# Kernel tuning notes

Hardware: AMD Instinct MI355X
Metric: run time of the kernel (lower is better)

## Reference

```python
import jax, jax.numpy as jnp
import numpy as np
from jax.scipy.special import gammaln, xlogy

B, T, C = 1, 1536, 1536
H, K, V = 8, 64, 192   # heads, key size per head, value size per head (C // H)
F = 192                # num_relative_position_features (C // H)
LN_EPS = 1e-3          # keras LayerNormalization default


def _layer_norm(x, g, b):
    mu = jnp.mean(x, axis=-1, keepdims=True)
    var = jnp.var(x, axis=-1, keepdims=True)
    return (x - mu) * jax.lax.rsqrt(var + LN_EPS) * g + b


def _positional_features(positions, feature_size, seq_length):
    # 3 symmetric basis classes x 2 (symmetric + sign-asymmetric) = 6 components
    n = feature_size // 6
    ap = jnp.abs(positions)[:, None]  # [L, 1]
    # exponential half-life decay
    half_life = (2.0 ** np.linspace(3.0, np.log2(seq_length), n)).astype(np.float32)
    f_exp = jnp.exp(ap * (-(np.log(2.0) / half_life))[None, :].astype(np.float32))
    # central mask
    widths = (2.0 ** np.arange(1, n + 1) - 1.0).astype(np.float32)
    f_cm = (widths[None, :] > ap).astype(jnp.float32)
    # gamma pdf bumps
    stddev = seq_length / (2.0 * n)
    mean = np.linspace(seq_length / n, float(seq_length), n)
    conc = ((mean / stddev) ** 2).astype(np.float32)
    rate = (mean / stddev ** 2).astype(np.float32)
    log_unnorm = xlogy(conc - 1.0, ap) - rate * ap
    log_norm = (gammaln(conc) - conc * np.log(rate)).astype(np.float32)
    prob = jnp.exp(log_unnorm - log_norm) + 1e-8
    f_g = prob / jnp.max(prob, axis=1, keepdims=True)
    emb = jnp.concatenate([f_exp, f_cm, f_g], axis=-1)          # [L, F/2]
    emb = jnp.concatenate([emb, jnp.sign(positions)[:, None] * emb], axis=-1)
    return emb                                                   # [L, F]


def _relative_shift(x):
    # TransformerXL shift: [B,H,T,2T-1] -> [B,H,T,T]
    b, h, t1, t2 = x.shape
    x = jnp.pad(x, ((0, 0), (0, 0), (0, 0), (1, 0)))
    x = x.reshape(b, h, t2 + 1, t1)[:, :, 1:, :].reshape(b, h, t1, t2)
    return x[..., :(t2 + 1) // 2]


def _forward(x, ln1_g, ln1_b, ln2_g, ln2_b, Wq, Wk, Wv, Wr, Wo, bo,
             r_w_bias, r_r_bias, W1, b1, W2, b2):
    Bv, Tv, Cv = x.shape
    # --- multi-head attention with relative positions ---
    xn = _layer_norm(x, ln1_g, ln1_b)
    q = (xn @ Wq).reshape(Bv, Tv, H, K).transpose(0, 2, 1, 3) * (K ** -0.5)
    k = (xn @ Wk).reshape(Bv, Tv, H, K).transpose(0, 2, 1, 3)
    v = (xn @ Wv).reshape(Bv, Tv, H, V).transpose(0, 2, 1, 3)
    content = jnp.einsum('bhqk,bhmk->bhqm', q + r_w_bias, k)     # [B,H,T,T]
    distances = jnp.arange(-Tv + 1, Tv, dtype=jnp.float32)       # [2T-1]
    pos = _positional_features(distances, F, Tv)                 # [2T-1, F]
    r_k = (pos @ Wr).reshape(2 * Tv - 1, H, K).transpose(1, 0, 2)
    rel = jnp.einsum('bhqk,hmk->bhqm', q + r_r_bias, r_k)        # [B,H,T,2T-1]
    logits = content + _relative_shift(rel)
    attn = jax.nn.softmax(logits, axis=-1)
    o = jnp.einsum('bhqm,bhmv->bhqv', attn, v)
    o = o.transpose(0, 2, 1, 3).reshape(Bv, Tv, H * V) @ Wo + bo
    y = x + o
    # --- MLP ---
    yn = _layer_norm(y, ln2_g, ln2_b)
    h1 = jax.nn.relu(yn @ W1 + b1)
    return y + h1 @ W2 + b2


def setup_inputs() -> dict:
    key = jax.random.key(0)
    ks = jax.random.split(key, 10)
    nrm = lambda i, shape, s=0.02: jax.random.normal(ks[i], shape, jnp.float32) * s
    return {
        'x': jax.random.normal(ks[0], (B, T, C), jnp.float32),
        'ln1_g': jnp.ones((C,), jnp.float32), 'ln1_b': jnp.zeros((C,), jnp.float32),
        'ln2_g': jnp.ones((C,), jnp.float32), 'ln2_b': jnp.zeros((C,), jnp.float32),
        'Wq': nrm(1, (C, H * K)), 'Wk': nrm(2, (C, H * K)), 'Wv': nrm(3, (C, H * V)),
        'Wr': nrm(4, (F, H * K)), 'Wo': nrm(5, (H * V, C)),
        'bo': jnp.zeros((C,), jnp.float32),
        'r_w_bias': nrm(6, (1, H, 1, K), 0.1), 'r_r_bias': nrm(7, (1, H, 1, K), 0.1),
        'W1': nrm(8, (C, 2 * C)), 'b1': jnp.zeros((2 * C,), jnp.float32),
        'W2': nrm(9, (2 * C, C)), 'b2': jnp.zeros((C,), jnp.float32),
    }


def reference(x, ln1_g, ln1_b, ln2_g, ln2_b, Wq, Wk, Wv, Wr, Wo, bo,
              r_w_bias, r_r_bias, W1, b1, W2, b2):
    return _forward(x, ln1_g, ln1_b, ln2_g, ln2_b, Wq, Wk, Wv, Wr, Wo, bo,
                    r_w_bias, r_r_bias, W1, b1, W2, b2)
```

## Files before the change

kernel.cpp:

```cpp
#include <hip/hip_runtime.h>
#include <math.h>

#define TT 1536
#define CC 1536
#define NH 8
#define KD 64
#define VD 192
#define FD 192

typedef short bf16x8 __attribute__((ext_vector_type(8)));
typedef float f32x4 __attribute__((ext_vector_type(4)));

__device__ inline unsigned short f2bf(float x) {
    unsigned u = __float_as_uint(x);
    u += 0x7FFF + ((u >> 16) & 1);
    return (unsigned short)(u >> 16);
}
__device__ inline float bf2f(unsigned short b) {
    return __uint_as_float(((unsigned)b) << 16);
}
__device__ inline void gload16(const void* g, void* l) {
    __builtin_amdgcn_global_load_lds(
        (const __attribute__((address_space(1))) unsigned int*)g,
        (__attribute__((address_space(3))) unsigned int*)l, 16, 0, 0);
}
__device__ inline int swzo(int row, int chunk) { return (chunk ^ (row & 7)) << 3; }

template<int N> __device__ inline void vmwait() {
    if constexpr (N == 0)      asm volatile("s_waitcnt vmcnt(0)" ::: "memory");
    else if constexpr (N == 4) asm volatile("s_waitcnt vmcnt(4)" ::: "memory");
    else if constexpr (N == 6) asm volatile("s_waitcnt vmcnt(6)" ::: "memory");
    else                       asm volatile("s_waitcnt vmcnt(8)" ::: "memory");
}

__global__ __launch_bounds__(256)
void ln_kernel(const float* __restrict__ x, const float* __restrict__ g,
               const float* __restrict__ b, unsigned short* __restrict__ out)
{
    int row = blockIdx.x;
    int tid = threadIdx.x;
    const float* xr = x + (size_t)row * CC;
    unsigned short* orow = out + (size_t)row * CC;

    float vals[6];
    float s = 0.f, ss = 0.f;
#pragma unroll
    for (int i = 0; i < 6; i++) {
        float v = xr[tid + i * 256];
        vals[i] = v;
        s += v; ss += v * v;
    }
    __shared__ float red[256], red2[256];
    red[tid] = s; red2[tid] = ss;
    __syncthreads();
    for (int off = 128; off > 0; off >>= 1) {
        if (tid < off) { red[tid] += red[tid + off]; red2[tid] += red2[tid + off]; }
        __syncthreads();
    }
    float mean = red[0] * (1.f / CC);
    float var  = red2[0] * (1.f / CC) - mean * mean;
    float rstd = rsqrtf(fmaxf(var, 0.f) + 1e-3f);
#pragma unroll
    for (int i = 0; i < 6; i++) {
        int c = tid + i * 256;
        orow[c] = f2bf((vals[i] - mean) * rstd * g[c] + b[c]);
    }
}

struct WCD { const float* W; unsigned short* Wt; int Kw, Nw, t0; };
struct WCP { WCD e[7]; };

__global__ __launch_bounds__(256)
void wconv_all(WCP p)
{
    __shared__ float t[32][33];
    int bid = blockIdx.x;
    int i = 0;
#pragma unroll
    for (int j = 1; j < 7; j++) if (bid >= p.e[j].t0) i = j;
    const float* W = p.e[i].W;
    unsigned short* Wt = p.e[i].Wt;
    int Kw = p.e[i].Kw, Nw = p.e[i].Nw;
    int local = bid - p.e[i].t0;
    int tpx = Nw >> 5;
    int n0 = (local % tpx) * 32, k0 = (local / tpx) * 32;

    int tid = threadIdx.x;
    int r = tid >> 3, c4 = (tid & 7) * 4;
    float4 v = *reinterpret_cast<const float4*>(&W[(size_t)(k0 + r) * Nw + n0 + c4]);
    t[r][c4 + 0] = v.x; t[r][c4 + 1] = v.y; t[r][c4 + 2] = v.z; t[r][c4 + 3] = v.w;
    __syncthreads();
    ushort4 pk;
    pk.x = f2bf(t[c4 + 0][r]);
    pk.y = f2bf(t[c4 + 1][r]);
    pk.z = f2bf(t[c4 + 2][r]);
    pk.w = f2bf(t[c4 + 3][r]);
    *reinterpret_cast<ushort4*>(&Wt[(size_t)(n0 + r) * Kw + k0 + c4]) = pk;
}

__global__ __launch_bounds__(128)
void pos_kernel(unsigned short* __restrict__ pos)
{
    int l = blockIdx.x;
    int tid = threadIdx.x;
    float p = (float)(l - (TT - 1));
    float ap = fabsf(p);
    float sgn = (p > 0.f) ? 1.f : ((p < 0.f) ? -1.f : 0.f);

    __shared__ float gp[32];
    __shared__ float gmax_s;
    if (tid < 32) {
        int j = tid;
        double conc = 4.0 * (double)(j + 1) * (double)(j + 1);
        double rate = (double)(j + 1) / 12.0;
        double log_norm = lgamma(conc) - conc * log(rate);
        double prob;
        if (ap == 0.f) prob = 1e-8;
        else prob = exp((conc - 1.0) * log((double)ap) - rate * (double)ap - log_norm) + 1e-8;
        gp[j] = (float)prob;
    }
    __syncthreads();
    if (tid == 0) {
        float m = gp[0];
        for (int j = 1; j < 32; j++) m = fmaxf(m, gp[j]);
        gmax_s = m;
    }
    __syncthreads();
    if (tid < 96) {
        int cls = tid / 32, j = tid % 32;
        float val;
        if (cls == 0) {
            double step = (10.584962500721156 - 3.0) / 31.0;
            double hl = exp2(3.0 + j * step);
            val = (float)exp(-(double)ap * 0.6931471805599453 / hl);
        } else if (cls == 1) {
            float width = exp2f((float)(j + 1)) - 1.f;
            val = (width > ap) ? 1.f : 0.f;
        } else {
            val = gp[j] / gmax_s;
        }
        pos[(size_t)l * FD + tid] = f2bf(val);
        pos[(size_t)l * FD + 96 + tid] = f2bf(sgn * val);
    }
}

template<int TM, int TN>
__global__ __launch_bounds__(256)
void gemm_bf16(const unsigned short* __restrict__ A,
               const unsigned short* __restrict__ Bt,
               void* __restrict__ Cv, unsigned short* __restrict__ C2,
               unsigned short* __restrict__ C3,
               int M, int N, int K, int lda, int ldb, int ldc,
               long sA, long sB, long sC,
               float alpha, const float* __restrict__ bias,
               const float* __restrict__ bias2,
               const float* __restrict__ resid,
               int mode, int relu, int head_ndiv, int xm)
{
    constexpr int WM = TM / 2, WN = TN / 2;
    constexpr int MF = WM / 16, NF = WN / 16;
    constexpr int LPT = TM / 32 + TN / 32;
    __shared__ unsigned short lA[2][TM * 64];
    __shared__ unsigned short lB[2][TN * 64];

    int tid = threadIdx.x;
    int w = tid >> 6, l = tid & 63;

    int gx = gridDim.x, gy = gridDim.y;
    int d = blockIdx.y * gx + blockIdx.x;
    int bx, by;
    if (xm) {
        int xn = 8 / xm;
        int cm = gy / xm, cn = gx / xn;
        int xcd = d & 7, local = d >> 3;
        int bxl = local / cm, byl = local % cm;
        by = (xcd / xn) * cm + byl;
        bx = (xcd % xn) * cn + bxl;
    } else {
        int nwg = gx * gy;
        int work = d;
        if ((nwg & 7) == 0) work = (d & 7) * (nwg >> 3) + (d >> 3);
        bx = work % gx;
        by = work / gx;
    }

    int n0 = bx * TN;
    int m0 = by * TM;
    if (head_ndiv) {
        A += (size_t)(n0 / head_ndiv) * sA;
    } else {
        A  += (size_t)blockIdx.z * sA;
        Bt += (size_t)blockIdx.z * sB;
    }
    int R0 = (w & 1) * WM, C0 = (w >> 1) * WN;
    int lrow = l >> 3;
    int lsw = ((l & 7) ^ lrow) << 3;
    int l15 = l & 15, lg = l >> 4;

    f32x4 acc[MF][NF] = {};

    const int NSTEP = K >> 6;

    auto STAGE = [&](int t, int buf) {
        int k0 = t << 6;
#pragma unroll
        for (int q = 0; q < TM / 32; q++) {
            int r0 = w * (TM / 4) + q * 8;
            gload16(A + (size_t)(m0 + r0 + lrow) * lda + k0 + lsw, &lA[buf][r0 * 64]);
        }
#pragma unroll
        for (int q = 0; q < TN / 32; q++) {
            int r0 = w * (TN / 4) + q * 8;
            gload16(Bt + (size_t)(n0 + r0 + lrow) * ldb + k0 + lsw, &lB[buf][r0 * 64]);
        }
    };

    STAGE(0, 0);

    int cur = 0;
    for (int t = 0; t < NSTEP; ++t) {
        if (t + 1 < NSTEP) {
            STAGE(t + 1, cur ^ 1);
            vmwait<LPT>();
        } else {
            vmwait<0>();
        }
        __builtin_amdgcn_s_barrier();
        __builtin_amdgcn_sched_barrier(0);

#pragma unroll
        for (int kk = 0; kk < 2; kk++) {
            int ch = kk * 4 + lg;
            bf16x8 av[MF], bv[NF];
#pragma unroll
            for (int m = 0; m < MF; m++) {
                int row = R0 + m * 16 + l15;
                av[m] = *(const bf16x8*)&lA[cur][row * 64 + swzo(row, ch)];
            }
#pragma unroll
            for (int n = 0; n < NF; n++) {
                int row = C0 + n * 16 + l15;
                bv[n] = *(const bf16x8*)&lB[cur][row * 64 + swzo(row, ch)];
            }
#pragma unroll
            for (int m = 0; m < MF; m++)
#pragma unroll
                for (int n = 0; n < NF; n++)
                    acc[m][n] = __builtin_amdgcn_mfma_f32_16x16x32_bf16(av[m], bv[n], acc[m][n], 0, 0, 0);
        }
        __builtin_amdgcn_s_barrier();
        cur ^= 1;
    }

    int rb = m0 + R0 + lg * 4;
    int cb = n0 + C0 + l15;

    if (mode == 4) {
        unsigned short* qw = (unsigned short*)Cv;
#pragma unroll
        for (int m = 0; m < MF; m++) {
            int rowb = rb + m * 16;
#pragma unroll
            for (int n = 0; n < NF; n++) {
                int col = cb + n * 16;
                if (col < 512) {
#pragma unroll
                    for (int reg = 0; reg < 4; reg++) {
                        int row = rowb + reg;
                        float v = alpha * acc[m][n][reg];
                        qw[(size_t)row * 512 + col] = f2bf(v + bias[col]);
                        C2[(size_t)row * 512 + col] = f2bf(v + bias2[col]);
                    }
                } else if (col < 1024) {
                    unsigned short* kb = C3;
#pragma unroll
                    for (int reg = 0; reg < 4; reg++)
                        kb[(size_t)(rowb + reg) * 512 + col - 512] = f2bf(acc[m][n][reg]);
                } else {
                    unsigned short* vT = (unsigned short*)(void*)(C3 + (size_t)1536 * 512);
                    int vc = col - 1024;
                    ushort4 pk;
                    pk.x = f2bf(acc[m][n][0]);
                    pk.y = f2bf(acc[m][n][1]);
                    pk.z = f2bf(acc[m][n][2]);
                    pk.w = f2bf(acc[m][n][3]);
                    *reinterpret_cast<ushort4*>(&vT[(size_t)vc * 1536 + rowb]) = pk;
                }
            }
        }
        return;
    }

#pragma unroll
    for (int m = 0; m < MF; m++) {
#pragma unroll
        for (int n = 0; n < NF; n++) {
            int col = cb + n * 16;
            if (col >= N) continue;
            float bs = bias ? bias[col] : 0.f;
#pragma unroll
            for (int reg = 0; reg < 4; reg++) {
                int row = rb + m * 16 + reg;
                if (row >= M) continue;
                float v = alpha * acc[m][n][reg] + bs;
                if (resid) v += resid[(size_t)row * ldc + col];
                if (relu)  v = fmaxf(v, 0.f);
                if (mode == 1) {
                    unsigned short* C = (unsigned short*)Cv + (size_t)blockIdx.z * sC;
                    C[(size_t)row * ldc + col] = f2bf(v);
                } else {
                    float* C = (float*)Cv + (size_t)blockIdx.z * sC;
                    C[(size_t)row * ldc + col] = v;
                }
            }
        }
    }
}

__global__ __launch_bounds__(256)
void logits_mfma(const unsigned short* __restrict__ qw,
                 const unsigned short* __restrict__ qr,
                 const unsigned short* __restrict__ kmat,
                 const unsigned short* __restrict__ rk,
                 unsigned short* __restrict__ out)
{
    __shared__ unsigned short pool[3 * 64 * 64 + 128 * 64];
    unsigned short* lQw = pool;
    unsigned short* lQr = pool + 64 * 64;
    unsigned short* lK  = pool + 2 * 64 * 64;
    unsigned short* lR  = pool + 3 * 64 * 64;
    unsigned short* lC2 = pool;

    int j0 = blockIdx.x * 64;
    int i0 = blockIdx.y * 64;
    int h  = blockIdx.z;
    int tid = threadIdx.x;
    int w = tid >> 6, l = tid & 63;
    int lrow = l >> 3;
    int lsw = ((l & 7) ^ lrow) << 3;
    int l15 = l & 15, lg = l >> 4;
    int obase = j0 - i0 + 1472;

#pragma unroll
    for (int q = 0; q < 2; q++) {
        int r0 = w * 16 + q * 8;
        gload16(qw   + (size_t)(i0 + r0 + lrow) * (NH * KD) + h * KD + lsw, &lQw[r0 * 64]);
        gload16(qr   + (size_t)(i0 + r0 + lrow) * (NH * KD) + h * KD + lsw, &lQr[r0 * 64]);
        gload16(kmat + (size_t)(j0 + r0 + lrow) * (NH * KD) + h * KD + lsw, &lK [r0 * 64]);
    }
#pragma unroll
    for (int q = 0; q < 4; q++) {
        int r0 = w * 32 + q * 8;
        gload16(rk + (size_t)(obase + r0 + lrow) * (NH * KD) + h * KD + lsw, &lR[r0 * 64]);
    }
    __syncthreads();

    f32x4 acc1[4] = {};
    f32x4 acc2[8] = {};
#pragma unroll
    for (int kk = 0; kk < 2; kk++) {
        int ch = kk * 4 + lg;
        int qrow = 16 * w + l15;
        bf16x8 av  = *(const bf16x8*)&lQw[qrow * 64 + swzo(qrow, ch)];
        bf16x8 arv = *(const bf16x8*)&lQr[qrow * 64 + swzo(qrow, ch)];
#pragma unroll
        for (int n = 0; n < 4; n++) {
            int row = n * 16 + l15;
            bf16x8 bv = *(const bf16x8*)&lK[row * 64 + swzo(row, ch)];
            acc1[n] = __builtin_amdgcn_mfma_f32_16x16x32_bf16(av, bv, acc1[n], 0, 0, 0);
        }
#pragma unroll
        for (int n = 0; n < 8; n++) {
            int row = n * 16 + l15;
            bf16x8 rv = *(const bf16x8*)&lR[row * 64 + swzo(row, ch)];
            acc2[n] = __builtin_amdgcn_mfma_f32_16x16x32_bf16(arv, rv, acc2[n], 0, 0, 0);
        }
    }
    __syncthreads();

#pragma unroll
    for (int n = 0; n < 8; n++)
#pragma unroll
        for (int reg = 0; reg < 4; reg++)
            lC2[(16 * w + lg * 4 + reg) * 128 + n * 16 + l15] = f2bf(acc2[n][reg]);
    __syncthreads();

#pragma unroll
    for (int n = 0; n < 4; n++) {
#pragma unroll
        for (int reg = 0; reg < 4; reg++) {
            int u = 16 * w + lg * 4 + reg;
            int v = n * 16 + l15;
            float val = acc1[n][reg] + bf2f(lC2[u * 128 + 63 + v - u]);
            out[((size_t)h * TT + i0 + u) * TT + j0 + v] = f2bf(val);
        }
    }
}

__global__ __launch_bounds__(256)
void softmax_bf16(unsigned short* __restrict__ P)
{
    int r = blockIdx.x;
    int tid = threadIdx.x;
    unsigned* row = (unsigned*)(P + (size_t)r * TT);

    unsigned u[3]; float v[6];
#pragma unroll
    for (int i = 0; i < 3; i++) u[i] = row[tid + i * 256];
    float m = -1e30f;
#pragma unroll
    for (int i = 0; i < 3; i++) {
        v[2 * i]     = bf2f((unsigned short)(u[i] & 0xFFFF));
        v[2 * i + 1] = bf2f((unsigned short)(u[i] >> 16));
        m = fmaxf(m, fmaxf(v[2 * i], v[2 * i + 1]));
    }
    __shared__ float red[256];
    red[tid] = m; __syncthreads();
    for (int off = 128; off > 0; off >>= 1) {
        if (tid < off) red[tid] = fmaxf(red[tid], red[tid + off]);
        __syncthreads();
    }
    m = red[0];
    __syncthreads();
    float s = 0.f;
#pragma unroll
    for (int i = 0; i < 6; i++) { v[i] = __expf(v[i] - m); s += v[i]; }
    red[tid] = s; __syncthreads();
    for (int off = 128; off > 0; off >>= 1) {
        if (tid < off) red[tid] += red[tid + off];
        __syncthreads();
    }
    float inv = 1.f / red[0];
#pragma unroll
    for (int i = 0; i < 3; i++)
        row[tid + i * 256] = (unsigned)f2bf(v[2 * i] * inv)
                           | ((unsigned)f2bf(v[2 * i + 1] * inv) << 16);
}

extern "C" void kernel_launch(void* const* d_in, const int* in_sizes, int n_in,
                              void* d_out, int out_size, void* d_ws, size_t ws_size,
                              hipStream_t stream)
{
    const float* x     = (const float*)d_in[0];
    const float* ln1_g = (const float*)d_in[1];
    const float* ln1_b = (const float*)d_in[2];
    const float* ln2_g = (const float*)d_in[3];
    const float* ln2_b = (const float*)d_in[4];
    const float* Wq    = (const float*)d_in[5];
    const float* Wk    = (const float*)d_in[6];
    const float* Wv    = (const float*)d_in[7];
    const float* Wr    = (const float*)d_in[8];
    const float* Wo    = (const float*)d_in[9];
    const float* bo    = (const float*)d_in[10];
    const float* rwb   = (const float*)d_in[11];
    const float* rrb   = (const float*)d_in[12];
    const float* W1    = (const float*)d_in[13];
    const float* b1    = (const float*)d_in[14];
    const float* W2    = (const float*)d_in[15];
    const float* b2    = (const float*)d_in[16];
    float* out = (float*)d_out;

    char* w8 = (char*)d_ws;
    unsigned short* xnb  = (unsigned short*)(w8 + 0);
    unsigned short* qwb  = (unsigned short*)(w8 + 4718592);
    unsigned short* qrb  = (unsigned short*)(w8 + 6291456);
    unsigned short* kbb  = (unsigned short*)(w8 + 7864320);
    unsigned short* vTb  = (unsigned short*)(w8 + 9437184);
    unsigned short* posb = (unsigned short*)(w8 + 14155776);
    unsigned short* rkb  = (unsigned short*)(w8 + 15335424);
    unsigned short* Pb   = (unsigned short*)(w8 + 18481152);
    unsigned short* ob   = (unsigned short*)(w8 + 56229888);
    float*          yb   = (float*)        (w8 + 60948480);
    unsigned short* WqkvT= (unsigned short*)(w8 + 70385664);
    unsigned short* WrT  = (unsigned short*)(w8 + 78249984);
    unsigned short* WoT  = (unsigned short*)(w8 + 78446592);
    unsigned short* W1T  = (unsigned short*)(w8 + 83165184);
    unsigned short* W2T  = (unsigned short*)(w8 + 92602368);
    unsigned short* h1b  = Pb;
    unsigned short* ynb  = xnb;

    WCP wp;
    wp.e[0] = { Wq, WqkvT,                       1536, 512,      0 };
    wp.e[1] = { Wk, WqkvT + (size_t)512 * 1536,  1536, 512,    768 };
    wp.e[2] = { Wv, WqkvT + (size_t)1024 * 1536, 1536, 1536,  1536 };
    wp.e[3] = { Wr, WrT,                          192, 512,   3840 };
    wp.e[4] = { Wo, WoT,                         1536, 1536,  3936 };
    wp.e[5] = { W1, W1T,                         1536, 3072,  6240 };
    wp.e[6] = { W2, W2T,                         3072, 1536, 10848 };
    wconv_all<<<15456, 256, 0, stream>>>(wp);

    ln_kernel<<<TT, 256, 0, stream>>>(x, ln1_g, ln1_b, xnb);
    pos_kernel<<<2 * TT - 1, 128, 0, stream>>>(posb);

    gemm_bf16<64, 128><<<dim3(20, 24, 1), 256, 0, stream>>>(xnb, WqkvT, qwb, qrb, kbb,
        1536, 2560, 1536, 1536, 1536, 0, 0, 0, 0,
        0.125f, rwb, rrb, nullptr, 4, 0, 0, 2);

    gemm_bf16<64, 128><<<dim3(4, 48, 1), 256, 0, stream>>>(posb, WrT, rkb, nullptr, nullptr,
        3071, 512, 192, 192, 192, 512, 0, 0, 0,
        1.f, nullptr, nullptr, nullptr, 1, 0, 0, 2);

    logits_mfma<<<dim3(24, 24, 8), 256, 0, stream>>>(qwb, qrb, kbb, rkb, Pb);
    softmax_bf16<<<NH * TT, 256, 0, stream>>>(Pb);

    gemm_bf16<64, 64><<<dim3(24, 24, 1), 256, 0, stream>>>(Pb, vTb, ob, nullptr, nullptr,
        1536, 1536, 1536, 1536, 1536, 1536, (long)TT * TT, 0, 0,
        1.f, nullptr, nullptr, nullptr, 1, 0, VD, 2);

    gemm_bf16<64, 64><<<dim3(24, 24, 1), 256, 0, stream>>>(ob, WoT, yb, nullptr, nullptr,
        1536, 1536, 1536, 1536, 1536, 1536, 0, 0, 0,
        1.f, bo, nullptr, x, 0, 0, 0, 2);

    ln_kernel<<<TT, 256, 0, stream>>>(yb, ln2_g, ln2_b, ynb);

    gemm_bf16<64, 128><<<dim3(24, 24, 1), 256, 0, stream>>>(ynb, W1T, h1b, nullptr, nullptr,
        1536, 3072, 1536, 1536, 1536, 3072, 0, 0, 0,
        1.f, b1, nullptr, nullptr, 1, 1, 0, 2);

    gemm_bf16<64, 64><<<dim3(24, 24, 1), 256, 0, stream>>>(h1b, W2T, out, nullptr, nullptr,
        1536, 1536, 3072, 3072, 3072, 1536, 0, 0, 0,
        1.f, b2, nullptr, yb, 0, 0, 0, 4);
}
```

Baseline: 217.9 us.

## Add triple-buffered LDS pipeline to bf16 GEMM and shrink all tiles to 64x64

```diff
diff --git a/kernel.cpp b/kernel.cpp
--- a/kernel.cpp
+++ b/kernel.cpp
@@ -27,10 +27,12 @@
 __device__ inline int swzo(int row, int chunk) { return (chunk ^ (row & 7)) << 3; }
 
 template<int N> __device__ inline void vmwait() {
-    if constexpr (N == 0)      asm volatile("s_waitcnt vmcnt(0)" ::: "memory");
-    else if constexpr (N == 4) asm volatile("s_waitcnt vmcnt(4)" ::: "memory");
-    else if constexpr (N == 6) asm volatile("s_waitcnt vmcnt(6)" ::: "memory");
-    else                       asm volatile("s_waitcnt vmcnt(8)" ::: "memory");
+    if constexpr (N == 0)       asm volatile("s_waitcnt vmcnt(0)" ::: "memory");
+    else if constexpr (N == 4)  asm volatile("s_waitcnt vmcnt(4)" ::: "memory");
+    else if constexpr (N == 6)  asm volatile("s_waitcnt vmcnt(6)" ::: "memory");
+    else if constexpr (N == 8)  asm volatile("s_waitcnt vmcnt(8)" ::: "memory");
+    else if constexpr (N == 12) asm volatile("s_waitcnt vmcnt(12)" ::: "memory");
+    else                        asm volatile("s_waitcnt vmcnt(0)" ::: "memory");
 }
 
 __global__ __launch_bounds__(256)
@@ -144,7 +146,7 @@
     }
 }
 
-template<int TM, int TN>
+template<int TM, int TN, int DEPTH>
 __global__ __launch_bounds__(256)
 void gemm_bf16(const unsigned short* __restrict__ A,
                const unsigned short* __restrict__ Bt,
@@ -160,8 +162,8 @@
     constexpr int WM = TM / 2, WN = TN / 2;
     constexpr int MF = WM / 16, NF = WN / 16;
     constexpr int LPT = TM / 32 + TN / 32;
-    __shared__ unsigned short lA[2][TM * 64];
-    __shared__ unsigned short lB[2][TN * 64];
+    __shared__ unsigned short lA[DEPTH][TM * 64];
+    __shared__ unsigned short lB[DEPTH][TN * 64];
 
     int tid = threadIdx.x;
     int w = tid >> 6, l = tid & 63;
@@ -216,11 +218,14 @@
     };
 
     STAGE(0, 0);
-
-    int cur = 0;
+    if (DEPTH >= 3 && NSTEP > 1) STAGE(1, 1);
+
     for (int t = 0; t < NSTEP; ++t) {
-        if (t + 1 < NSTEP) {
-            STAGE(t + 1, cur ^ 1);
+        int cur = t % DEPTH;
+        if (t + DEPTH - 1 < NSTEP) {
+            STAGE(t + DEPTH - 1, (t + DEPTH - 1) % DEPTH);
+            vmwait<(DEPTH - 1) * LPT>();
+        } else if (DEPTH >= 3 && t + 1 < NSTEP) {
             vmwait<LPT>();
         } else {
             vmwait<0>();
@@ -249,7 +254,6 @@
                     acc[m][n] = __builtin_amdgcn_mfma_f32_16x16x32_bf16(av[m], bv[n], acc[m][n], 0, 0, 0);
         }
         __builtin_amdgcn_s_barrier();
-        cur ^= 1;
     }
 
     int rb = m0 + R0 + lg * 4;
@@ -492,32 +496,32 @@
     ln_kernel<<<TT, 256, 0, stream>>>(x, ln1_g, ln1_b, xnb);
     pos_kernel<<<2 * TT - 1, 128, 0, stream>>>(posb);
 
-    gemm_bf16<64, 128><<<dim3(20, 24, 1), 256, 0, stream>>>(xnb, WqkvT, qwb, qrb, kbb,
+    gemm_bf16<64, 64, 3><<<dim3(40, 24, 1), 256, 0, stream>>>(xnb, WqkvT, qwb, qrb, kbb,
         1536, 2560, 1536, 1536, 1536, 0, 0, 0, 0,
         0.125f, rwb, rrb, nullptr, 4, 0, 0, 2);
 
-    gemm_bf16<64, 128><<<dim3(4, 48, 1), 256, 0, stream>>>(posb, WrT, rkb, nullptr, nullptr,
+    gemm_bf16<64, 64, 3><<<dim3(8, 48, 1), 256, 0, stream>>>(posb, WrT, rkb, nullptr, nullptr,
         3071, 512, 192, 192, 192, 512, 0, 0, 0,
         1.f, nullptr, nullptr, nullptr, 1, 0, 0, 2);
 
     logits_mfma<<<dim3(24, 24, 8), 256, 0, stream>>>(qwb, qrb, kbb, rkb, Pb);
     softmax_bf16<<<NH * TT, 256, 0, stream>>>(Pb);
 
-    gemm_bf16<64, 64><<<dim3(24, 24, 1), 256, 0, stream>>>(Pb, vTb, ob, nullptr, nullptr,
+    gemm_bf16<64, 64, 3><<<dim3(24, 24, 1), 256, 0, stream>>>(Pb, vTb, ob, nullptr, nullptr,
         1536, 1536, 1536, 1536, 1536, 1536, (long)TT * TT, 0, 0,
         1.f, nullptr, nullptr, nullptr, 1, 0, VD, 2);
 
-    gemm_bf16<64, 64><<<dim3(24, 24, 1), 256, 0, stream>>>(ob, WoT, yb, nullptr, nullptr,
+    gemm_bf16<64, 64, 3><<<dim3(24, 24, 1), 256, 0, stream>>>(ob, WoT, yb, nullptr, nullptr,
         1536, 1536, 1536, 1536, 1536, 1536, 0, 0, 0,
         1.f, bo, nullptr, x, 0, 0, 0, 2);
 
     ln_kernel<<<TT, 256, 0, stream>>>(yb, ln2_g, ln2_b, ynb);
 
-    gemm_bf16<64, 128><<<dim3(24, 24, 1), 256, 0, stream>>>(ynb, W1T, h1b, nullptr, nullptr,
+    gemm_bf16<64, 64, 3><<<dim3(48, 24, 1), 256, 0, stream>>>(ynb, W1T, h1b, nullptr, nullptr,
         1536, 3072, 1536, 1536, 1536, 3072, 0, 0, 0,
         1.f, b1, nullptr, nullptr, 1, 1, 0, 2);
 
-    gemm_bf16<64, 64><<<dim3(24, 24, 1), 256, 0, stream>>>(h1b, W2T, out, nullptr, nullptr,
+    gemm_bf16<64, 64, 3><<<dim3(24, 24, 1), 256, 0, stream>>>(h1b, W2T, out, nullptr, nullptr,
         1536, 1536, 3072, 3072, 3072, 1536, 0, 0, 0,
         1.f, b2, nullptr, yb, 0, 0, 0, 4);
 }
```

New measurement: 233.5 us. 7.1% more time.

## Merge prep kernels and use wave-per-row layernorm and softmax

Applied to the files above, without the earlier changes.

```diff
diff --git a/kernel.cpp b/kernel.cpp
--- a/kernel.cpp
+++ b/kernel.cpp
@@ -33,114 +33,139 @@
     else                       asm volatile("s_waitcnt vmcnt(8)" ::: "memory");
 }
 
+__device__ inline void ln_row(const float* __restrict__ x,
+                              const float* __restrict__ g,
+                              const float* __restrict__ b,
+                              unsigned short* __restrict__ out,
+                              int row, int lane)
+{
+    const float* xr = x + (size_t)row * CC;
+    unsigned short* orow = out + (size_t)row * CC;
+
+    float4 V[6];
+    float s = 0.f, ss = 0.f;
+#pragma unroll
+    for (int c = 0; c < 6; c++) {
+        V[c] = *reinterpret_cast<const float4*>(&xr[c * 256 + lane * 4]);
+        s  += V[c].x + V[c].y + V[c].z + V[c].w;
+        ss += V[c].x * V[c].x + V[c].y * V[c].y + V[c].z * V[c].z + V[c].w * V[c].w;
+    }
+#pragma unroll
+    for (int off = 32; off; off >>= 1) {
+        s  += __shfl_xor(s, off);
+        ss += __shfl_xor(ss, off);
+    }
+    float mean = s * (1.f / CC);
+    float var  = ss * (1.f / CC) - mean * mean;
+    float rstd = rsqrtf(fmaxf(var, 0.f) + 1e-3f);
+#pragma unroll
+    for (int c = 0; c < 6; c++) {
+        float4 G = *reinterpret_cast<const float4*>(&g[c * 256 + lane * 4]);
+        float4 B = *reinterpret_cast<const float4*>(&b[c * 256 + lane * 4]);
+        ushort4 pk;
+        pk.x = f2bf((V[c].x - mean) * rstd * G.x + B.x);
+        pk.y = f2bf((V[c].y - mean) * rstd * G.y + B.y);
+        pk.z = f2bf((V[c].z - mean) * rstd * G.z + B.z);
+        pk.w = f2bf((V[c].w - mean) * rstd * G.w + B.w);
+        *reinterpret_cast<ushort4*>(&orow[c * 256 + lane * 4]) = pk;
+    }
+}
+
 __global__ __launch_bounds__(256)
 void ln_kernel(const float* __restrict__ x, const float* __restrict__ g,
                const float* __restrict__ b, unsigned short* __restrict__ out)
 {
-    int row = blockIdx.x;
-    int tid = threadIdx.x;
-    const float* xr = x + (size_t)row * CC;
-    unsigned short* orow = out + (size_t)row * CC;
-
-    float vals[6];
-    float s = 0.f, ss = 0.f;
-#pragma unroll
-    for (int i = 0; i < 6; i++) {
-        float v = xr[tid + i * 256];
-        vals[i] = v;
-        s += v; ss += v * v;
-    }
-    __shared__ float red[256], red2[256];
-    red[tid] = s; red2[tid] = ss;
-    __syncthreads();
-    for (int off = 128; off > 0; off >>= 1) {
-        if (tid < off) { red[tid] += red[tid + off]; red2[tid] += red2[tid + off]; }
-        __syncthreads();
-    }
-    float mean = red[0] * (1.f / CC);
-    float var  = red2[0] * (1.f / CC) - mean * mean;
-    float rstd = rsqrtf(fmaxf(var, 0.f) + 1e-3f);
-#pragma unroll
-    for (int i = 0; i < 6; i++) {
-        int c = tid + i * 256;
-        orow[c] = f2bf((vals[i] - mean) * rstd * g[c] + b[c]);
-    }
+    int wid = threadIdx.x >> 6, lane = threadIdx.x & 63;
+    ln_row(x, g, b, out, blockIdx.x * 4 + wid, lane);
 }
 
 struct WCD { const float* W; unsigned short* Wt; int Kw, Nw, t0; };
 struct WCP { WCD e[7]; };
+#define WCONV_BLKS 15456
+#define LN1_BLKS   384
+#define POS_BLKS   (2 * TT - 1)
 
 __global__ __launch_bounds__(256)
-void wconv_all(WCP p)
-{
-    __shared__ float t[32][33];
+void prep_all(WCP p, const float* __restrict__ x,
+              const float* __restrict__ ln1_g, const float* __restrict__ ln1_b,
+              unsigned short* __restrict__ xnb, unsigned short* __restrict__ pos)
+{
     int bid = blockIdx.x;
-    int i = 0;
-#pragma unroll
-    for (int j = 1; j < 7; j++) if (bid >= p.e[j].t0) i = j;
-    const float* W = p.e[i].W;
-    unsigned short* Wt = p.e[i].Wt;
-    int Kw = p.e[i].Kw, Nw = p.e[i].Nw;
-    int local = bid - p.e[i].t0;
-    int tpx = Nw >> 5;
-    int n0 = (local % tpx) * 32, k0 = (local / tpx) * 32;
-
     int tid = threadIdx.x;
-    int r = tid >> 3, c4 = (tid & 7) * 4;
-    float4 v = *reinterpret_cast<const float4*>(&W[(size_t)(k0 + r) * Nw + n0 + c4]);
-    t[r][c4 + 0] = v.x; t[r][c4 + 1] = v.y; t[r][c4 + 2] = v.z; t[r][c4 + 3] = v.w;
-    __syncthreads();
-    ushort4 pk;
-    pk.x = f2bf(t[c4 + 0][r]);
-    pk.y = f2bf(t[c4 + 1][r]);
-    pk.z = f2bf(t[c4 + 2][r]);
-    pk.w = f2bf(t[c4 + 3][r]);
-    *reinterpret_cast<ushort4*>(&Wt[(size_t)(n0 + r) * Kw + k0 + c4]) = pk;
-}
-
-__global__ __launch_bounds__(128)
-void pos_kernel(unsigned short* __restrict__ pos)
-{
-    int l = blockIdx.x;
-    int tid = threadIdx.x;
-    float p = (float)(l - (TT - 1));
-    float ap = fabsf(p);
-    float sgn = (p > 0.f) ? 1.f : ((p < 0.f) ? -1.f : 0.f);
-
-    __shared__ float gp[32];
-    __shared__ float gmax_s;
-    if (tid < 32) {
-        int j = tid;
-        double conc = 4.0 * (double)(j + 1) * (double)(j + 1);
-        double rate = (double)(j + 1) / 12.0;
-        double log_norm = lgamma(conc) - conc * log(rate);
-        double prob;
-        if (ap == 0.f) prob = 1e-8;
-        else prob = exp((conc - 1.0) * log((double)ap) - rate * (double)ap - log_norm) + 1e-8;
-        gp[j] = (float)prob;
-    }
-    __syncthreads();
-    if (tid == 0) {
-        float m = gp[0];
-        for (int j = 1; j < 32; j++) m = fmaxf(m, gp[j]);
-        gmax_s = m;
-    }
-    __syncthreads();
-    if (tid < 96) {
-        int cls = tid / 32, j = tid % 32;
-        float val;
-        if (cls == 0) {
-            double step = (10.584962500721156 - 3.0) / 31.0;
-            double hl = exp2(3.0 + j * step);
-            val = (float)exp(-(double)ap * 0.6931471805599453 / hl);
-        } else if (cls == 1) {
-            float width = exp2f((float)(j + 1)) - 1.f;
-            val = (width > ap) ? 1.f : 0.f;
-        } else {
-            val = gp[j] / gmax_s;
-        }
-        pos[(size_t)l * FD + tid] = f2bf(val);
-        pos[(size_t)l * FD + 96 + tid] = f2bf(sgn * val);
+
+    if (bid < WCONV_BLKS) {
+        __shared__ float t[32][33];
+        int i = 0;
+#pragma unroll
+        for (int j = 1; j < 7; j++) if (bid >= p.e[j].t0) i = j;
+        const float* W = p.e[i].W;
+        unsigned short* Wt = p.e[i].Wt;
+        int Kw = p.e[i].Kw, Nw = p.e[i].Nw;
+        int local = bid - p.e[i].t0;
+        int tpx = Nw >> 5;
+        int n0 = (local % tpx) * 32, k0 = (local / tpx) * 32;
+
+        int r = tid >> 3, c4 = (tid & 7) * 4;
+        float4 v = *reinterpret_cast<const float4*>(&W[(size_t)(k0 + r) * Nw + n0 + c4]);
+        t[r][c4 + 0] = v.x; t[r][c4 + 1] = v.y; t[r][c4 + 2] = v.z; t[r][c4 + 3] = v.w;
+        __syncthreads();
+        ushort4 pk;
+        pk.x = f2bf(t[c4 + 0][r]);
+        pk.y = f2bf(t[c4 + 1][r]);
+        pk.z = f2bf(t[c4 + 2][r]);
+        pk.w = f2bf(t[c4 + 3][r]);
+        *reinterpret_cast<ushort4*>(&Wt[(size_t)(n0 + r) * Kw + k0 + c4]) = pk;
+        return;
+    }
+
+    if (bid < WCONV_BLKS + LN1_BLKS) {
+        int grp = bid - WCONV_BLKS;
+        int wid = tid >> 6, lane = tid & 63;
+        ln_row(x, ln1_g, ln1_b, xnb, grp * 4 + wid, lane);
+        return;
+    }
+
+    {
+        int l = bid - (WCONV_BLKS + LN1_BLKS);
+        float pp = (float)(l - (TT - 1));
+        float ap = fabsf(pp);
+        float sgn = (pp > 0.f) ? 1.f : ((pp < 0.f) ? -1.f : 0.f);
+
+        __shared__ float gp[32];
+        __shared__ float gmax_s;
+        if (tid < 32) {
+            int j = tid;
+            double conc = 4.0 * (double)(j + 1) * (double)(j + 1);
+            double rate = (double)(j + 1) / 12.0;
+            double log_norm = lgamma(conc) - conc * log(rate);
+            double prob;
+            if (ap == 0.f) prob = 1e-8;
+            else prob = exp((conc - 1.0) * log((double)ap) - rate * (double)ap - log_norm) + 1e-8;
+            gp[j] = (float)prob;
+        }
+        __syncthreads();
+        if (tid == 0) {
+            float m = gp[0];
+            for (int j = 1; j < 32; j++) m = fmaxf(m, gp[j]);
+            gmax_s = m;
+        }
+        __syncthreads();
+        if (tid < 96) {
+            int cls = tid / 32, j = tid % 32;
+            float val;
+            if (cls == 0) {
+                double step = (10.584962500721156 - 3.0) / 31.0;
+                double hl = exp2(3.0 + j * step);
+                val = (float)exp(-(double)ap * 0.6931471805599453 / hl);
+            } else if (cls == 1) {
+                float width = exp2f((float)(j + 1)) - 1.f;
+                val = (width > ap) ? 1.f : 0.f;
+            } else {
+                val = gp[j] / gmax_s;
+            }
+            pos[(size_t)l * FD + tid] = f2bf(val);
+            pos[(size_t)l * FD + 96 + tid] = f2bf(sgn * val);
+        }
     }
 }
 
@@ -400,41 +425,43 @@
 __global__ __launch_bounds__(256)
 void softmax_bf16(unsigned short* __restrict__ P)
 {
-    int r = blockIdx.x;
-    int tid = threadIdx.x;
-    unsigned* row = (unsigned*)(P + (size_t)r * TT);
-
-    unsigned u[3]; float v[6];
-#pragma unroll
-    for (int i = 0; i < 3; i++) u[i] = row[tid + i * 256];
+    int wid = threadIdx.x >> 6, lane = threadIdx.x & 63;
+    size_t r = (size_t)blockIdx.x * 4 + wid;
+    unsigned* row = (unsigned*)(P + r * TT);
+
+    uint4 U[3];
+    float v[24];
     float m = -1e30f;
 #pragma unroll
-    for (int i = 0; i < 3; i++) {
-        v[2 * i]     = bf2f((unsigned short)(u[i] & 0xFFFF));
-        v[2 * i + 1] = bf2f((unsigned short)(u[i] >> 16));
-        m = fmaxf(m, fmaxf(v[2 * i], v[2 * i + 1]));
-    }
-    __shared__ float red[256];
-    red[tid] = m; __syncthreads();
-    for (int off = 128; off > 0; off >>= 1) {
-        if (tid < off) red[tid] = fmaxf(red[tid], red[tid + off]);
-        __syncthreads();
-    }
-    m = red[0];
-    __syncthreads();
+    for (int c = 0; c < 3; c++) {
+        U[c] = *reinterpret_cast<const uint4*>(&row[c * 256 + lane * 4]);
+        const unsigned* pd = (const unsigned*)&U[c];
+#pragma unroll
+        for (int d = 0; d < 4; d++) {
+            float lo = bf2f((unsigned short)(pd[d] & 0xFFFF));
+            float hi = bf2f((unsigned short)(pd[d] >> 16));
+            v[c * 8 + 2 * d]     = lo;
+            v[c * 8 + 2 * d + 1] = hi;
+            m = fmaxf(m, fmaxf(lo, hi));
+        }
+    }
+#pragma unroll
+    for (int off = 32; off; off >>= 1) m = fmaxf(m, __shfl_xor(m, off));
     float s = 0.f;
 #pragma unroll
-    for (int i = 0; i < 6; i++) { v[i] = __expf(v[i] - m); s += v[i]; }
-    red[tid] = s; __syncthreads();
-    for (int off = 128; off > 0; off >>= 1) {
-        if (tid < off) red[tid] += red[tid + off];
-        __syncthreads();
-    }
-    float inv = 1.f / red[0];
-#pragma unroll
-    for (int i = 0; i < 3; i++)
-        row[tid + i * 256] = (unsigned)f2bf(v[2 * i] * inv)
-                           | ((unsigned)f2bf(v[2 * i + 1] * inv) << 16);
+    for (int i = 0; i < 24; i++) { v[i] = __expf(v[i] - m); s += v[i]; }
+#pragma unroll
+    for (int off = 32; off; off >>= 1) s += __shfl_xor(s, off);
+    float inv = 1.f / s;
+#pragma unroll
+    for (int c = 0; c < 3; c++) {
+        unsigned* pd = (unsigned*)&U[c];
+#pragma unroll
+        for (int d = 0; d < 4; d++)
+            pd[d] = (unsigned)f2bf(v[c * 8 + 2 * d] * inv)
+                  | ((unsigned)f2bf(v[c * 8 + 2 * d + 1] * inv) << 16);
+        *reinterpret_cast<uint4*>(&row[c * 256 + lane * 4]) = U[c];
+    }
 }
 
 extern "C" void kernel_launch(void* const* d_in, const int* in_sizes, int n_in,
@@ -487,10 +514,8 @@
     wp.e[4] = { Wo, WoT,                         1536, 1536,  3936 };
     wp.e[5] = { W1, W1T,                         1536, 3072,  6240 };
     wp.e[6] = { W2, W2T,                         3072, 1536, 10848 };
-    wconv_all<<<15456, 256, 0, stream>>>(wp);
-
-    ln_kernel<<<TT, 256, 0, stream>>>(x, ln1_g, ln1_b, xnb);
-    pos_kernel<<<2 * TT - 1, 128, 0, stream>>>(posb);
+    prep_all<<<WCONV_BLKS + LN1_BLKS + POS_BLKS, 256, 0, stream>>>(
+        wp, x, ln1_g, ln1_b, xnb, posb);
 
     gemm_bf16<64, 128><<<dim3(20, 24, 1), 256, 0, stream>>>(xnb, WqkvT, qwb, qrb, kbb,
         1536, 2560, 1536, 1536, 1536, 0, 0, 0, 0,
@@ -501,7 +526,7 @@
         1.f, nullptr, nullptr, nullptr, 1, 0, 0, 2);
 
     logits_mfma<<<dim3(24, 24, 8), 256, 0, stream>>>(qwb, qrb, kbb, rkb, Pb);
-    softmax_bf16<<<NH * TT, 256, 0, stream>>>(Pb);
+    softmax_bf16<<<NH * TT / 4, 256, 0, stream>>>(Pb);
 
     gemm_bf16<64, 64><<<dim3(24, 24, 1), 256, 0, stream>>>(Pb, vTb, ob, nullptr, nullptr,
         1536, 1536, 1536, 1536, 1536, 1536, (long)TT * TT, 0, 0,
@@ -511,7 +536,7 @@
         1536, 1536, 1536, 1536, 1536, 1536, 0, 0, 0,
         1.f, bo, nullptr, x, 0, 0, 0, 2);
 
-    ln_kernel<<<TT, 256, 0, stream>>>(yb, ln2_g, ln2_b, ynb);
+    ln_kernel<<<TT / 4, 256, 0, stream>>>(yb, ln2_g, ln2_b, ynb);
 
     gemm_bf16<64, 128><<<dim3(24, 24, 1), 256, 0, stream>>>(ynb, W1T, h1b, nullptr, nullptr,
         1536, 3072, 1536, 1536, 1536, 3072, 0, 0, 0,
```

Result: faster. 209.7 us (-3.8%).
